# Kernel tuning notes

Hardware: AMD Instinct MI355X
Metric: run time of the kernel (lower is better)

Reference implementation:

```python
import jax, jax.numpy as jnp
import numpy as np

B, C, H, W = 4, 256, 64, 64
TOPK = 3
RAT_S = 0.05  # rat_s passed in Corr.forward


def _zero_window_mask(h, w, rat_s=RAT_S):
    # mask[m, i, j] = 1 - gaussian centered at pixel m=(m//w, m%w); sigma=(h*rat_s, w*rat_s)
    sr, sc = h * rat_s, w * rat_s
    r = jnp.arange(h, dtype=jnp.float32)
    c = jnp.arange(w, dtype=jnp.float32)
    cent_r = jnp.repeat(r, w)  # [hw]
    cent_c = jnp.tile(c, h)    # [hw]
    g = (jnp.exp(-((r[None, :, None] - cent_r[:, None, None]) ** 2) / (2.0 * sr * sr))
         * jnp.exp(-((c[None, None, :] - cent_c[:, None, None]) ** 2) / (2.0 * sc * sc)))
    return (1.0 - g).reshape(h * w, h * w)


def setup_inputs() -> dict:
    key = jax.random.key(0)
    x = jax.random.normal(key, (B, C, H, W), dtype=jnp.float32)
    alpha = jnp.asarray(5.0, dtype=jnp.float32)  # learned scalar nn.Parameter
    return {"x": x, "alpha": alpha}


def reference(x, alpha):
    b, c, h, w = x.shape
    # F.normalize(x, p=2, dim=-3): L2-normalize channels with eps clamp
    nrm = jnp.linalg.norm(x, axis=1, keepdims=True)
    xn = x / jnp.maximum(nrm, 1e-12)
    xf = xn.reshape(b, c, h * w)
    # correlation GEMM: [b, hw, hw]
    aff = jnp.einsum('bcm,bcn->bmn', xf, xf)
    aff = aff * _zero_window_mask(h, w)[None]
    s = aff * alpha
    xc = jax.nn.softmax(s, axis=-1) * jax.nn.softmax(s, axis=-2)
    # topk over the source-pixel dim (dim=-3 of [b, hw, h, w])
    xc = xc.reshape(b, h * w, h, w).transpose(0, 2, 3, 1)  # [b, h, w, hw]
    val, _ = jax.lax.top_k(xc, TOPK)                        # [b, h, w, k]
    return val.transpose(0, 3, 1, 2)                        # [b, k, h, w]
```

## Files before the change

kernel.cpp:

```cpp
#include <hip/hip_runtime.h>
#include <hip/hip_bf16.h>


#define HW 4096
#define CDIM 256
#define INV2S2 0.048828125f
#define NEGINF -1e30f

typedef __bf16 bf16;
typedef __attribute__((ext_vector_type(8))) __bf16 bf16x8;
typedef __attribute__((ext_vector_type(4))) float f32x4;

#define GAS __attribute__((address_space(1)))
#define LAS __attribute__((address_space(3)))

__device__ __forceinline__ void ins3(float v, float& t0, float& t1, float& t2) {
    float n0 = fmaxf(t0, v);
    float n1 = __builtin_amdgcn_fmed3f(t0, t1, v);
    float n2 = __builtin_amdgcn_fmed3f(t1, t2, v);
    t0 = n0; t1 = n1; t2 = n2;
}

__device__ __forceinline__ void decode_tri(int t, int& mt, int& nt) {
    int m = (int)((sqrtf(8.f * (float)t + 1.f) - 1.f) * 0.5f);
    while ((m + 1) * (m + 2) / 2 <= t) ++m;
    while (m * (m + 1) / 2 > t) --m;
    mt = m;
    nt = t - m * (m + 1) / 2;
}

__global__ __launch_bounds__(256) void corr_norm(const float* __restrict__ x,
                                                 bf16* __restrict__ xnT) {
    __shared__ float red[4][64];
    __shared__ float invn[64];
    __shared__ __align__(16) bf16 T[64][264];
    int tid = threadIdx.x;
    int pl = tid & 63, cg = tid >> 6;
    int P0 = blockIdx.x * 64;
    int P = P0 + pl;
    int b = P >> 12;
    int pix = P & 4095;
    const float* xb = x + ((size_t)(b * CDIM + cg * 64) << 12) + pix;
    float v[64];
    float ss = 0.f;
#pragma unroll
    for (int j = 0; j < 64; ++j) {
        v[j] = xb[(size_t)j << 12];
        ss += v[j] * v[j];
    }
    red[cg][pl] = ss;
    __syncthreads();
    if (tid < 64) {
        float s = red[0][tid] + red[1][tid] + red[2][tid] + red[3][tid];
        invn[tid] = 1.0f / fmaxf(sqrtf(s), 1e-12f);
    }
    __syncthreads();
    float inv = invn[pl];
#pragma unroll
    for (int j0 = 0; j0 < 64; j0 += 8) {
        bf16x8 pk;
#pragma unroll
        for (int j = 0; j < 8; ++j) pk[j] = (bf16)(v[j0 + j] * inv);
        *(bf16x8*)(&T[pl][cg * 64 + j0]) = pk;
    }
    __syncthreads();
#pragma unroll
    for (int it = 0; it < 8; ++it) {
        int p = it * 8 + (tid >> 5);
        int k = tid & 31;
        bf16x8 val = *(const bf16x8*)(&T[p][k * 8]);
        *(bf16x8*)(xnT + (size_t)(P0 + p) * CDIM + k * 8) = val;
    }
}

__device__ __forceinline__ void gemm_tile(const bf16* __restrict__ xb, int mbase, int nbase,
                                          bf16* As, bf16* Bs, f32x4 (&acc)[4][4]) {
    const int tid = threadIdx.x;
    const int wave = tid >> 6;
    const int lane = tid & 63;
    const int wm = wave >> 1, wn = wave & 1;
    const int l15 = lane & 15, quad = lane >> 4;
#pragma unroll
    for (int mi = 0; mi < 4; ++mi)
#pragma unroll
        for (int ni = 0; ni < 4; ++ni) acc[mi][ni] = (f32x4)0.f;

    auto issue = [&](int kk, int buf) {
#pragma unroll
        for (int r = 0; r < 2; ++r) {
            int idx = r * 256 + tid;
            int prow = idx >> 2;
            int sub = ((idx & 3) - (prow >> 1)) & 3;
            const bf16* gA = xb + ((size_t)(mbase + prow) << 8) + kk * 32 + (sub << 3);
            const bf16* gB = xb + ((size_t)(nbase + prow) << 8) + kk * 32 + (sub << 3);
            bf16* lA = As + buf * 4096 + ((r * 4 + wave) << 9);
            bf16* lB = Bs + buf * 4096 + ((r * 4 + wave) << 9);
            __builtin_amdgcn_global_load_lds((const GAS void*)gA, (LAS void*)lA, 16, 0, 0);
            __builtin_amdgcn_global_load_lds((const GAS void*)gB, (LAS void*)lB, 16, 0, 0);
        }
    };
    issue(0, 0);
    const int rslot = ((quad + (l15 >> 1)) & 3) * 8;
#pragma unroll
    for (int kk = 0; kk < 8; ++kk) {
        __syncthreads();
        if (kk < 7) issue(kk + 1, (kk + 1) & 1);
        int buf = kk & 1;
        bf16x8 af[4], bfr[4];
#pragma unroll
        for (int i = 0; i < 4; ++i) {
            af[i]  = *(const bf16x8*)(As + buf * 4096 + (wm * 64 + i * 16 + l15) * 32 + rslot);
            bfr[i] = *(const bf16x8*)(Bs + buf * 4096 + (wn * 64 + i * 16 + l15) * 32 + rslot);
        }
#pragma unroll
        for (int mi = 0; mi < 4; ++mi)
#pragma unroll
            for (int ni = 0; ni < 4; ++ni)
                acc[mi][ni] = __builtin_amdgcn_mfma_f32_16x16x32_bf16(af[mi], bfr[ni],
                                                                      acc[mi][ni], 0, 0, 0);
    }
}

__device__ __forceinline__ void build_ext(float* extw, int lane, int adr, float scale) {
    float fr2 = (float)(adr * adr);
#pragma unroll
    for (int h = 0; h < 2; ++h) {
        int j = lane + h * 64;
        float d = (float)(j - 63);
        extw[j] = scale * (1.f - __expf(-(fr2 + d * d) * INV2S2));
    }
}

__device__ __forceinline__ void load_etab(const float* extw_wave, int quad, int l15,
                                          float (&e)[7][4]) {
    const float* p = extw_wave + 63 + quad * 4 - l15;
#pragma unroll
    for (int dm = 0; dm < 7; ++dm)
#pragma unroll
        for (int r = 0; r < 4; ++r) e[dm][r] = p[(dm - 3) * 16 + r];
}

__global__ __launch_bounds__(256) void corr_rowsum(const bf16* __restrict__ xnT,
                                                   const float* __restrict__ alpha_p,
                                                   float* __restrict__ rpart) {
    __shared__ __align__(16) bf16 SH[16384];
    bf16* As = SH;
    bf16* Bs = SH + 8192;
    int tid = threadIdx.x;
    int lin = blockIdx.x;
    int xcd = lin & 7;
    int b = xcd >> 1;
    int t = ((lin >> 3) << 1) + (xcd & 1);
    int mt, nt;
    decode_tri(t, mt, nt);
    int mbase = mt * 128, nbase = nt * 128;
    int wave = tid >> 6, lane = tid & 63;
    int wm = wave >> 1, wn = wave & 1, l15 = lane & 15, quad = lane >> 4;
    int rowi = (mbase + wm * 64) >> 6;
    int coli = (nbase + wn * 64) >> 6;
    int adr = rowi - coli; if (adr < 0) adr = -adr;
    float alpha = alpha_p[0];

    f32x4 acc[4][4];
    gemm_tile(xnT + ((size_t)b << 20), mbase, nbase, As, Bs, acc);

    float* F = (float*)SH;
    float* ext  = F;
    float* rbuf = F + 512;
    float* cbuf = F + 768;
    build_ext(ext + wave * 128, lane, adr, alpha);
    float e[7][4];
    load_etab(ext + wave * 128, quad, l15, e);

    float colpart[4] = {0.f, 0.f, 0.f, 0.f};
#pragma unroll
    for (int mi = 0; mi < 4; ++mi) {
#pragma unroll
        for (int r = 0; r < 4; ++r) {
            float ssum = 0.f;
#pragma unroll
            for (int ni = 0; ni < 4; ++ni) {
                float s = e[mi - ni + 3][r] * acc[mi][ni][r];
                float ev = __expf(s);
                ssum += ev;
                colpart[ni] += ev;
            }
            ssum += __shfl_xor(ssum, 1);
            ssum += __shfl_xor(ssum, 2);
            ssum += __shfl_xor(ssum, 4);
            ssum += __shfl_xor(ssum, 8);
            if (l15 == 0) rbuf[wn * 128 + wm * 64 + mi * 16 + quad * 4 + r] = ssum;
        }
    }
#pragma unroll
    for (int ni = 0; ni < 4; ++ni) {
        float c = colpart[ni];
        c += __shfl_xor(c, 16);
        c += __shfl_xor(c, 32);
        if (quad == 0) cbuf[wm * 128 + wn * 64 + ni * 16 + l15] = c;
    }
    __syncthreads();
    if (tid < 128) {
        rpart[(size_t)((b * 32 + mt) * 32 + nt) * 128 + tid] = rbuf[tid] + rbuf[128 + tid];
    } else if (mt != nt) {
        int j = tid - 128;
        rpart[(size_t)((b * 32 + nt) * 32 + mt) * 128 + j] = cbuf[j] + cbuf[128 + j];
    }
}

__global__ __launch_bounds__(256) void corr_recip(const float* __restrict__ rpart,
                                                  float* __restrict__ ism,
                                                  float* __restrict__ lsm) {
    int i = blockIdx.x * 256 + threadIdx.x;
    if (i >= 4 * HW) return;
    int b = i >> 12, gr = i & 4095, s = gr >> 7, j = gr & 127;
    const float* base = rpart + (size_t)((b * 32 + s) * 32) * 128 + j;
    float sum = 0.f;
#pragma unroll
    for (int sl = 0; sl < 32; ++sl) sum += base[sl * 128];
    ism[i] = 1.0f / sum;
    lsm[i] = -__logf(sum);
}

__global__ __launch_bounds__(256) void corr_topk(const bf16* __restrict__ xnT,
                                                 const float* __restrict__ alpha_p,
                                                 const float* __restrict__ lsm,
                                                 float* __restrict__ wtop) {
    __shared__ __align__(16) bf16 SH[16384];
    bf16* As = SH;
    bf16* Bs = SH + 8192;
    int tid = threadIdx.x;
    int lin = blockIdx.x;
    int xcd = lin & 7;
    int b = xcd >> 1;
    int t = ((lin >> 3) << 1) + (xcd & 1);
    int mt, nt;
    decode_tri(t, mt, nt);
    int mbase = mt * 128, nbase = nt * 128;
    int wave = tid >> 6, lane = tid & 63;
    int wm = wave >> 1, wn = wave & 1, l15 = lane & 15, quad = lane >> 4;
    int rowi = (mbase + wm * 64) >> 6;
    int coli = (nbase + wn * 64) >> 6;
    int adr = rowi - coli; if (adr < 0) adr = -adr;
    float a2 = 2.0f * alpha_p[0];

    f32x4 acc[4][4];
    gemm_tile(xnT + ((size_t)b << 20), mbase, nbase, As, Bs, acc);

    float* F = (float*)SH;
    float* ext  = F;
    float* mbuf = F + 512;
    float* rtop = F + 1280;
    build_ext(ext + wave * 128, lane, adr, a2);
    float e[7][4];
    load_etab(ext + wave * 128, quad, l15, e);

    float lr[4][4];
#pragma unroll
    for (int mi = 0; mi < 4; ++mi)
#pragma unroll
        for (int r = 0; r < 4; ++r)
            lr[mi][r] = lsm[(b << 12) + mbase + wm * 64 + mi * 16 + quad * 4 + r];
    float lc[4];
#pragma unroll
    for (int ni = 0; ni < 4; ++ni)
        lc[ni] = lsm[(b << 12) + nbase + wn * 64 + ni * 16 + l15];

#pragma unroll
    for (int ni = 0; ni < 4; ++ni) {
        float t0 = NEGINF, t1 = NEGINF, t2 = NEGINF;
#pragma unroll
        for (int mi = 0; mi < 4; ++mi) {
#pragma unroll
            for (int r = 0; r < 4; ++r) {
                float key = fmaf(e[mi - ni + 3][r], acc[mi][ni][r], lr[mi][r]);
                ins3(key, t0, t1, t2);
            }
        }
#pragma unroll
        for (int d = 16; d <= 32; d <<= 1) {
            float s0 = __shfl_xor(t0, d);
            float s1 = __shfl_xor(t1, d);
            float s2 = __shfl_xor(t2, d);
            ins3(s0, t0, t1, t2);
            ins3(s1, t0, t1, t2);
            ins3(s2, t0, t1, t2);
        }
        if (quad == 0) {
            int cl = wn * 64 + ni * 16 + l15;
            mbuf[(wm * 128 + cl) * 3 + 0] = t0;
            mbuf[(wm * 128 + cl) * 3 + 1] = t1;
            mbuf[(wm * 128 + cl) * 3 + 2] = t2;
        }
    }
    __syncthreads();

    if (mt != nt) {
#pragma unroll
        for (int mi = 0; mi < 4; ++mi) {
#pragma unroll
            for (int r = 0; r < 4; ++r) {
                float u0 = NEGINF, u1 = NEGINF, u2 = NEGINF;
#pragma unroll
                for (int ni = 0; ni < 4; ++ni) {
                    float key = fmaf(e[mi - ni + 3][r], acc[mi][ni][r], lc[ni]);
                    ins3(key, u0, u1, u2);
                }
                {
                    float s0 = __shfl_xor(u0, 8);
                    float s1 = __shfl_xor(u1, 8);
                    float s2 = __shfl_xor(u2, 8);
                    ins3(s0, u0, u1, u2);
                    ins3(s1, u0, u1, u2);
                    ins3(s2, u0, u1, u2);
                }
                if (l15 < 8) {
                    int row = wm * 64 + mi * 16 + quad * 4 + r;
                    int slot = wn * 8 + l15;
                    float* q = rtop + row * 51 + slot * 3;
                    q[0] = u0; q[1] = u1; q[2] = u2;
                }
            }
        }
    }
    __syncthreads();
    if (tid < 128) {
        float t0 = mbuf[tid * 3], t1 = mbuf[tid * 3 + 1], t2 = mbuf[tid * 3 + 2];
        ins3(mbuf[(128 + tid) * 3 + 0], t0, t1, t2);
        ins3(mbuf[(128 + tid) * 3 + 1], t0, t1, t2);
        ins3(mbuf[(128 + tid) * 3 + 2], t0, t1, t2);
        size_t o = ((size_t)((b * 32 + nt) * 32 + mt) * 128 + tid) * 3;
        wtop[o] = t0;
        wtop[o + 1] = t1;
        wtop[o + 2] = t2;
        if (mt != nt) {
            float v0 = NEGINF, v1 = NEGINF, v2 = NEGINF;
            const float* q = rtop + tid * 51;
#pragma unroll
            for (int sl = 0; sl < 16; ++sl) {
                ins3(q[sl * 3 + 0], v0, v1, v2);
                ins3(q[sl * 3 + 1], v0, v1, v2);
                ins3(q[sl * 3 + 2], v0, v1, v2);
            }
            size_t o2 = ((size_t)((b * 32 + mt) * 32 + nt) * 128 + tid) * 3;
            wtop[o2] = v0;
            wtop[o2 + 1] = v1;
            wtop[o2 + 2] = v2;
        }
    }
}

__global__ __launch_bounds__(256) void corr_merge(const float* __restrict__ wtop,
                                                  const float* __restrict__ ism,
                                                  float* __restrict__ out) {
    int idx = blockIdx.x * 256 + threadIdx.x;
    if (idx >= 4 * HW) return;
    int b = idx >> 12, col = idx & 4095;
    int strip = col >> 7, j = col & 127;
    const float* base = wtop + ((size_t)((b * 32 + strip) * 32) * 128 + j) * 3;
    float t0 = NEGINF, t1 = NEGINF, t2 = NEGINF;
    for (int sl = 0; sl < 32; ++sl) {
        const float* q = base + (size_t)sl * 128 * 3;
        ins3(q[0], t0, t1, t2);
        ins3(q[1], t0, t1, t2);
        ins3(q[2], t0, t1, t2);
    }
    float ismc = ism[idx];
    out[((b * 3 + 0) << 12) + col] = __expf(t0) * ismc;
    out[((b * 3 + 1) << 12) + col] = __expf(t1) * ismc;
    out[((b * 3 + 2) << 12) + col] = __expf(t2) * ismc;
}

extern "C" void kernel_launch(void* const* d_in, const int* in_sizes, int n_in,
                              void* d_out, int out_size, void* d_ws, size_t ws_size,
                              hipStream_t stream) {
    const float* x = (const float*)d_in[0];
    const float* alpha = (const float*)d_in[1];
    float* out = (float*)d_out;
    char* ws = (char*)d_ws;
    bf16* xnT = (bf16*)ws;
    float* ism = (float*)(ws + (8u << 20));
    float* lsm = (float*)(ws + (8u << 20) + (64u << 10));
    float* rpart = (float*)(ws + (8u << 20) + (128u << 10));
    float* wtop  = (float*)(ws + (8u << 20) + (128u << 10));

    corr_norm<<<256, 256, 0, stream>>>(x, xnT);
    corr_rowsum<<<528 * 4, 256, 0, stream>>>(xnT, alpha, rpart);
    corr_recip<<<64, 256, 0, stream>>>(rpart, ism, lsm);
    corr_topk<<<528 * 4, 256, 0, stream>>>(xnT, alpha, lsm, wtop);
    corr_merge<<<64, 256, 0, stream>>>(wtop, ism, out);
}
```

Before: 155.0 us.

## Fuse five kernels into one persistent kernel with global atomic barriers

```diff
diff --git a/kernel.cpp b/kernel.cpp
--- a/kernel.cpp
+++ b/kernel.cpp
@@ -6,6 +6,9 @@
 #define CDIM 256
 #define INV2S2 0.048828125f
 #define NEGINF -1e30f
+#define NTILE 528
+#define NWORK_GEMM (NTILE * 4)
+#define GRID 512
 
 typedef __bf16 bf16;
 typedef __attribute__((ext_vector_type(8))) __bf16 bf16x8;
@@ -19,6 +22,18 @@
     float n1 = __builtin_amdgcn_fmed3f(t0, t1, v);
     float n2 = __builtin_amdgcn_fmed3f(t1, t2, v);
     t0 = n0; t1 = n1; t2 = n2;
+}
+
+__device__ __forceinline__ void gbarrier(int* cnt, int target) {
+    __syncthreads();
+    if (threadIdx.x == 0) {
+        __threadfence();
+        __hip_atomic_fetch_add(cnt, 1, __ATOMIC_RELEASE, __HIP_MEMORY_SCOPE_AGENT);
+        while (__hip_atomic_load(cnt, __ATOMIC_ACQUIRE, __HIP_MEMORY_SCOPE_AGENT) < target)
+            __builtin_amdgcn_s_sleep(8);
+        __threadfence();
+    }
+    __syncthreads();
 }
 
 __device__ __forceinline__ void decode_tri(int t, int& mt, int& nt) {
@@ -27,50 +42,6 @@
     while (m * (m + 1) / 2 > t) --m;
     mt = m;
     nt = t - m * (m + 1) / 2;
-}
-
-__global__ __launch_bounds__(256) void corr_norm(const float* __restrict__ x,
-                                                 bf16* __restrict__ xnT) {
-    __shared__ float red[4][64];
-    __shared__ float invn[64];
-    __shared__ __align__(16) bf16 T[64][264];
-    int tid = threadIdx.x;
-    int pl = tid & 63, cg = tid >> 6;
-    int P0 = blockIdx.x * 64;
-    int P = P0 + pl;
-    int b = P >> 12;
-    int pix = P & 4095;
-    const float* xb = x + ((size_t)(b * CDIM + cg * 64) << 12) + pix;
-    float v[64];
-    float ss = 0.f;
-#pragma unroll
-    for (int j = 0; j < 64; ++j) {
-        v[j] = xb[(size_t)j << 12];
-        ss += v[j] * v[j];
-    }
-    red[cg][pl] = ss;
-    __syncthreads();
-    if (tid < 64) {
-        float s = red[0][tid] + red[1][tid] + red[2][tid] + red[3][tid];
-        invn[tid] = 1.0f / fmaxf(sqrtf(s), 1e-12f);
-    }
-    __syncthreads();
-    float inv = invn[pl];
-#pragma unroll
-    for (int j0 = 0; j0 < 64; j0 += 8) {
-        bf16x8 pk;
-#pragma unroll
-        for (int j = 0; j < 8; ++j) pk[j] = (bf16)(v[j0 + j] * inv);
-        *(bf16x8*)(&T[pl][cg * 64 + j0]) = pk;
-    }
-    __syncthreads();
-#pragma unroll
-    for (int it = 0; it < 8; ++it) {
-        int p = it * 8 + (tid >> 5);
-        int k = tid & 31;
-        bf16x8 val = *(const bf16x8*)(&T[p][k * 8]);
-        *(bf16x8*)(xnT + (size_t)(P0 + p) * CDIM + k * 8) = val;
-    }
 }
 
 __device__ __forceinline__ void gemm_tile(const bf16* __restrict__ xb, int mbase, int nbase,
@@ -140,14 +111,64 @@
         for (int r = 0; r < 4; ++r) e[dm][r] = p[(dm - 3) * 16 + r];
 }
 
-__global__ __launch_bounds__(256) void corr_rowsum(const bf16* __restrict__ xnT,
-                                                   const float* __restrict__ alpha_p,
-                                                   float* __restrict__ rpart) {
-    __shared__ __align__(16) bf16 SH[16384];
+__device__ __forceinline__ void norm_phase(int wid, const float* __restrict__ x,
+                                           bf16* __restrict__ xnT, bf16* SH) {
+    float* F = (float*)SH;
+    float* red  = F;
+    float* invn = F + 256;
+    bf16* T = SH + 4096;
+    int tid = threadIdx.x;
+    int pl = tid & 63, cg = tid >> 6;
+    int P0 = wid * 64;
+    int P = P0 + pl;
+    int b = P >> 12;
+    int pix = P & 4095;
+    const float* xb = x + ((size_t)(b * CDIM + cg * 64) << 12) + pix;
+    float v[64];
+    float ss = 0.f;
+#pragma unroll
+    for (int j = 0; j < 64; ++j) {
+        v[j] = xb[(size_t)j << 12];
+        ss += v[j] * v[j];
+    }
+    red[cg * 64 + pl] = ss;
+    __syncthreads();
+    if (tid < 64) {
+        float s = red[tid] + red[64 + tid] + red[128 + tid] + red[192 + tid];
+        invn[tid] = 1.0f / fmaxf(sqrtf(s), 1e-12f);
+    }
+    __syncthreads();
+    float inv = invn[pl];
+#pragma unroll
+    for (int h = 0; h < 2; ++h) {
+        if ((cg >> 1) == h) {
+            int base = (cg & 1) * 64;
+#pragma unroll
+            for (int j0 = 0; j0 < 64; j0 += 8) {
+                bf16x8 pk;
+#pragma unroll
+                for (int j = 0; j < 8; ++j) pk[j] = (bf16)(v[j0 + j] * inv);
+                *(bf16x8*)(T + pl * 136 + base + j0) = pk;
+            }
+        }
+        __syncthreads();
+#pragma unroll
+        for (int it = 0; it < 4; ++it) {
+            int p = it * 16 + (tid >> 4);
+            int k = tid & 15;
+            bf16x8 val = *(const bf16x8*)(T + p * 136 + k * 8);
+            *(bf16x8*)(xnT + (size_t)(P0 + p) * CDIM + h * 128 + k * 8) = val;
+        }
+        __syncthreads();
+    }
+}
+
+__device__ __forceinline__ void rowsum_phase(int lin, const bf16* __restrict__ xnT,
+                                             const float* __restrict__ alpha_p,
+                                             float* __restrict__ rpart, bf16* SH) {
     bf16* As = SH;
     bf16* Bs = SH + 8192;
     int tid = threadIdx.x;
-    int lin = blockIdx.x;
     int xcd = lin & 7;
     int b = xcd >> 1;
     int t = ((lin >> 3) << 1) + (xcd & 1);
@@ -206,13 +227,12 @@
         int j = tid - 128;
         rpart[(size_t)((b * 32 + nt) * 32 + mt) * 128 + j] = cbuf[j] + cbuf[128 + j];
     }
-}
-
-__global__ __launch_bounds__(256) void corr_recip(const float* __restrict__ rpart,
-                                                  float* __restrict__ ism,
-                                                  float* __restrict__ lsm) {
-    int i = blockIdx.x * 256 + threadIdx.x;
-    if (i >= 4 * HW) return;
+    __syncthreads();
+}
+
+__device__ __forceinline__ void recip_phase(int wid, const float* __restrict__ rpart,
+                                            float* __restrict__ ism, float* __restrict__ lsm) {
+    int i = wid * 256 + threadIdx.x;
     int b = i >> 12, gr = i & 4095, s = gr >> 7, j = gr & 127;
     const float* base = rpart + (size_t)((b * 32 + s) * 32) * 128 + j;
     float sum = 0.f;
@@ -222,15 +242,13 @@
     lsm[i] = -__logf(sum);
 }
 
-__global__ __launch_bounds__(256) void corr_topk(const bf16* __restrict__ xnT,
-                                                 const float* __restrict__ alpha_p,
-                                                 const float* __restrict__ lsm,
-                                                 float* __restrict__ wtop) {
-    __shared__ __align__(16) bf16 SH[16384];
+__device__ __forceinline__ void topk_phase(int lin, const bf16* __restrict__ xnT,
+                                           const float* __restrict__ alpha_p,
+                                           const float* __restrict__ lsm,
+                                           float* __restrict__ wtop, bf16* SH) {
     bf16* As = SH;
     bf16* Bs = SH + 8192;
     int tid = threadIdx.x;
-    int lin = blockIdx.x;
     int xcd = lin & 7;
     int b = xcd >> 1;
     int t = ((lin >> 3) << 1) + (xcd & 1);
@@ -348,13 +366,13 @@
             wtop[o2 + 2] = v2;
         }
     }
-}
-
-__global__ __launch_bounds__(256) void corr_merge(const float* __restrict__ wtop,
-                                                  const float* __restrict__ ism,
-                                                  float* __restrict__ out) {
-    int idx = blockIdx.x * 256 + threadIdx.x;
-    if (idx >= 4 * HW) return;
+    __syncthreads();
+}
+
+__device__ __forceinline__ void merge_phase(int wid, const float* __restrict__ wtop,
+                                            const float* __restrict__ ism,
+                                            float* __restrict__ out) {
+    int idx = wid * 256 + threadIdx.x;
     int b = idx >> 12, col = idx & 4095;
     int strip = col >> 7, j = col & 127;
     const float* base = wtop + ((size_t)((b * 32 + strip) * 32) * 128 + j) * 3;
@@ -369,6 +387,27 @@
     out[((b * 3 + 0) << 12) + col] = __expf(t0) * ismc;
     out[((b * 3 + 1) << 12) + col] = __expf(t1) * ismc;
     out[((b * 3 + 2) << 12) + col] = __expf(t2) * ismc;
+}
+
+__global__ __launch_bounds__(256, 2) void corr_all(const float* __restrict__ x,
+                                                   const float* __restrict__ alpha_p,
+                                                   bf16* __restrict__ xnT,
+                                                   float* __restrict__ rpart,
+                                                   float* __restrict__ ism,
+                                                   float* __restrict__ lsm,
+                                                   float* __restrict__ wtop,
+                                                   float* __restrict__ out,
+                                                   int* __restrict__ cnt) {
+    __shared__ __align__(16) bf16 SH[16384];
+    for (int w = blockIdx.x; w < 256; w += GRID) norm_phase(w, x, xnT, SH);
+    gbarrier(cnt, 1 * GRID);
+    for (int w = blockIdx.x; w < NWORK_GEMM; w += GRID) rowsum_phase(w, xnT, alpha_p, rpart, SH);
+    gbarrier(cnt, 2 * GRID);
+    for (int w = blockIdx.x; w < 64; w += GRID) recip_phase(w, rpart, ism, lsm);
+    gbarrier(cnt, 3 * GRID);
+    for (int w = blockIdx.x; w < NWORK_GEMM; w += GRID) topk_phase(w, xnT, alpha_p, lsm, wtop, SH);
+    gbarrier(cnt, 4 * GRID);
+    for (int w = blockIdx.x; w < 64; w += GRID) merge_phase(w, wtop, ism, out);
 }
 
 extern "C" void kernel_launch(void* const* d_in, const int* in_sizes, int n_in,
@@ -383,10 +422,8 @@
     float* lsm = (float*)(ws + (8u << 20) + (64u << 10));
     float* rpart = (float*)(ws + (8u << 20) + (128u << 10));
     float* wtop  = (float*)(ws + (8u << 20) + (128u << 10));
-
-    corr_norm<<<256, 256, 0, stream>>>(x, xnT);
-    corr_rowsum<<<528 * 4, 256, 0, stream>>>(xnT, alpha, rpart);
-    corr_recip<<<64, 256, 0, stream>>>(rpart, ism, lsm);
-    corr_topk<<<528 * 4, 256, 0, stream>>>(xnT, alpha, lsm, wtop);
-    corr_merge<<<64, 256, 0, stream>>>(wtop, ism, out);
-}
+    int* cnt = (int*)(ws + (8u << 20) + (128u << 10) + (6u << 20));
+
+    hipMemsetAsync(cnt, 0, 64, stream);
+    corr_all<<<GRID, 256, 0, stream>>>(x, alpha, xnT, rpart, ism, lsm, wtop, out, cnt);
+}
```

Result: slower. 460.1 us (+196.9%).

## Fuse row-sum reciprocal and top-k merge into GEMM kernels via last-block atomic counters

Applied to the files above, without the earlier changes.

```diff
diff --git a/kernel.cpp b/kernel.cpp
--- a/kernel.cpp
+++ b/kernel.cpp
@@ -6,6 +6,7 @@
 #define CDIM 256
 #define INV2S2 0.048828125f
 #define NEGINF -1e30f
+#define NTILE 528
 
 typedef __bf16 bf16;
 typedef __attribute__((ext_vector_type(8))) __bf16 bf16x8;
@@ -142,8 +143,12 @@
 
 __global__ __launch_bounds__(256) void corr_rowsum(const bf16* __restrict__ xnT,
                                                    const float* __restrict__ alpha_p,
-                                                   float* __restrict__ rpart) {
+                                                   float* __restrict__ rpart,
+                                                   float* __restrict__ ism,
+                                                   float* __restrict__ lsm,
+                                                   int* __restrict__ cnt) {
     __shared__ __align__(16) bf16 SH[16384];
+    __shared__ int fin0, fin1;
     bf16* As = SH;
     bf16* Bs = SH + 8192;
     int tid = threadIdx.x;
@@ -206,27 +211,54 @@
         int j = tid - 128;
         rpart[(size_t)((b * 32 + nt) * 32 + mt) * 128 + j] = cbuf[j] + cbuf[128 + j];
     }
-}
-
-__global__ __launch_bounds__(256) void corr_recip(const float* __restrict__ rpart,
-                                                  float* __restrict__ ism,
-                                                  float* __restrict__ lsm) {
-    int i = blockIdx.x * 256 + threadIdx.x;
-    if (i >= 4 * HW) return;
-    int b = i >> 12, gr = i & 4095, s = gr >> 7, j = gr & 127;
-    const float* base = rpart + (size_t)((b * 32 + s) * 32) * 128 + j;
-    float sum = 0.f;
-#pragma unroll
-    for (int sl = 0; sl < 32; ++sl) sum += base[sl * 128];
-    ism[i] = 1.0f / sum;
-    lsm[i] = -__logf(sum);
+    __syncthreads();
+    if (tid == 0) {
+        __threadfence();
+        int oa = __hip_atomic_fetch_add(&cnt[b * 32 + mt], 1, __ATOMIC_RELAXED,
+                                        __HIP_MEMORY_SCOPE_AGENT);
+        int f0 = (oa == 31);
+        int f1 = 0;
+        if (mt != nt) {
+            int ob = __hip_atomic_fetch_add(&cnt[b * 32 + nt], 1, __ATOMIC_RELAXED,
+                                            __HIP_MEMORY_SCOPE_AGENT);
+            f1 = (ob == 31);
+        }
+        if (f0 | f1) __threadfence();
+        fin0 = f0;
+        fin1 = f1;
+    }
+    __syncthreads();
+    if (tid < 128) {
+        if (fin0) {
+            int i = (b << 12) + mt * 128 + tid;
+            const float* base = rpart + (size_t)((b * 32 + mt) * 32) * 128 + tid;
+            float sum = 0.f;
+#pragma unroll
+            for (int sl = 0; sl < 32; ++sl) sum += base[sl * 128];
+            ism[i] = 1.0f / sum;
+            lsm[i] = -__logf(sum);
+        }
+        if (fin1) {
+            int i = (b << 12) + nt * 128 + tid;
+            const float* base = rpart + (size_t)((b * 32 + nt) * 32) * 128 + tid;
+            float sum = 0.f;
+#pragma unroll
+            for (int sl = 0; sl < 32; ++sl) sum += base[sl * 128];
+            ism[i] = 1.0f / sum;
+            lsm[i] = -__logf(sum);
+        }
+    }
 }
 
 __global__ __launch_bounds__(256) void corr_topk(const bf16* __restrict__ xnT,
                                                  const float* __restrict__ alpha_p,
                                                  const float* __restrict__ lsm,
-                                                 float* __restrict__ wtop) {
+                                                 const float* __restrict__ ism,
+                                                 float* __restrict__ wtop,
+                                                 float* __restrict__ out,
+                                                 int* __restrict__ cnt) {
     __shared__ __align__(16) bf16 SH[16384];
+    __shared__ int fin0, fin1;
     bf16* As = SH;
     bf16* Bs = SH + 8192;
     int tid = threadIdx.x;
@@ -348,27 +380,44 @@
             wtop[o2 + 2] = v2;
         }
     }
-}
-
-__global__ __launch_bounds__(256) void corr_merge(const float* __restrict__ wtop,
-                                                  const float* __restrict__ ism,
-                                                  float* __restrict__ out) {
-    int idx = blockIdx.x * 256 + threadIdx.x;
-    if (idx >= 4 * HW) return;
-    int b = idx >> 12, col = idx & 4095;
-    int strip = col >> 7, j = col & 127;
-    const float* base = wtop + ((size_t)((b * 32 + strip) * 32) * 128 + j) * 3;
-    float t0 = NEGINF, t1 = NEGINF, t2 = NEGINF;
-    for (int sl = 0; sl < 32; ++sl) {
-        const float* q = base + (size_t)sl * 128 * 3;
-        ins3(q[0], t0, t1, t2);
-        ins3(q[1], t0, t1, t2);
-        ins3(q[2], t0, t1, t2);
-    }
-    float ismc = ism[idx];
-    out[((b * 3 + 0) << 12) + col] = __expf(t0) * ismc;
-    out[((b * 3 + 1) << 12) + col] = __expf(t1) * ismc;
-    out[((b * 3 + 2) << 12) + col] = __expf(t2) * ismc;
+    __syncthreads();
+    if (tid == 0) {
+        __threadfence();
+        int oa = __hip_atomic_fetch_add(&cnt[b * 32 + nt], 1, __ATOMIC_RELAXED,
+                                        __HIP_MEMORY_SCOPE_AGENT);
+        int f0 = (oa == 31);
+        int f1 = 0;
+        if (mt != nt) {
+            int ob = __hip_atomic_fetch_add(&cnt[b * 32 + mt], 1, __ATOMIC_RELAXED,
+                                            __HIP_MEMORY_SCOPE_AGENT);
+            f1 = (ob == 31);
+        }
+        if (f0 | f1) __threadfence();
+        fin0 = f0;
+        fin1 = f1;
+    }
+    __syncthreads();
+    if (tid < 128) {
+        for (int pass = 0; pass < 2; ++pass) {
+            int s = pass == 0 ? nt : mt;
+            int go = pass == 0 ? fin0 : fin1;
+            if (!go) continue;
+            int idx = (b << 12) + s * 128 + tid;
+            const float* base = wtop + ((size_t)((b * 32 + s) * 32) * 128 + tid) * 3;
+            float t0 = NEGINF, t1 = NEGINF, t2 = NEGINF;
+            for (int sl = 0; sl < 32; ++sl) {
+                const float* q = base + (size_t)sl * 128 * 3;
+                ins3(q[0], t0, t1, t2);
+                ins3(q[1], t0, t1, t2);
+                ins3(q[2], t0, t1, t2);
+            }
+            float ismc = ism[idx];
+            int col = s * 128 + tid;
+            out[((b * 3 + 0) << 12) + col] = __expf(t0) * ismc;
+            out[((b * 3 + 1) << 12) + col] = __expf(t1) * ismc;
+            out[((b * 3 + 2) << 12) + col] = __expf(t2) * ismc;
+        }
+    }
 }
 
 extern "C" void kernel_launch(void* const* d_in, const int* in_sizes, int n_in,
@@ -383,10 +432,11 @@
     float* lsm = (float*)(ws + (8u << 20) + (64u << 10));
     float* rpart = (float*)(ws + (8u << 20) + (128u << 10));
     float* wtop  = (float*)(ws + (8u << 20) + (128u << 10));
-
+    int* cntA = (int*)(ws + (8u << 20) + (128u << 10) + (6u << 20));
+    int* cntB = cntA + 128;
+
+    hipMemsetAsync(cntA, 0, 256 * sizeof(int), stream);
     corr_norm<<<256, 256, 0, stream>>>(x, xnT);
-    corr_rowsum<<<528 * 4, 256, 0, stream>>>(xnT, alpha, rpart);
-    corr_recip<<<64, 256, 0, stream>>>(rpart, ism, lsm);
-    corr_topk<<<528 * 4, 256, 0, stream>>>(xnT, alpha, lsm, wtop);
-    corr_merge<<<64, 256, 0, stream>>>(wtop, ism, out);
-}
+    corr_rowsum<<<NTILE * 4, 256, 0, stream>>>(xnT, alpha, rpart, ism, lsm, cntA);
+    corr_topk<<<NTILE * 4, 256, 0, stream>>>(xnT, alpha, lsm, ism, wtop, out, cntB);
+}
```

Result: slower. 260.5 us (+68.1%).

## Store scaled scores as fp16 in rowsum pass and skip GEMM recompute in topk

Applied to the files above, without the earlier changes.

```diff
diff --git a/kernel.cpp b/kernel.cpp
--- a/kernel.cpp
+++ b/kernel.cpp
@@ -6,9 +6,12 @@
 #define CDIM 256
 #define INV2S2 0.048828125f
 #define NEGINF -1e30f
+#define NTILE 528
 
 typedef __bf16 bf16;
+typedef _Float16 f16;
 typedef __attribute__((ext_vector_type(8))) __bf16 bf16x8;
+typedef __attribute__((ext_vector_type(4))) _Float16 f16x4;
 typedef __attribute__((ext_vector_type(4))) float f32x4;
 
 #define GAS __attribute__((address_space(1)))
@@ -142,7 +145,9 @@
 
 __global__ __launch_bounds__(256) void corr_rowsum(const bf16* __restrict__ xnT,
                                                    const float* __restrict__ alpha_p,
-                                                   float* __restrict__ rpart) {
+                                                   float* __restrict__ rpart,
+                                                   f16* __restrict__ sbuf,
+                                                   int store_s2) {
     __shared__ __align__(16) bf16 SH[16384];
     bf16* As = SH;
     bf16* Bs = SH + 8192;
@@ -172,18 +177,27 @@
     float e[7][4];
     load_etab(ext + wave * 128, quad, l15, e);
 
+    const size_t tb = (size_t)(b * NTILE + t) * 16384;
     float colpart[4] = {0.f, 0.f, 0.f, 0.f};
 #pragma unroll
     for (int mi = 0; mi < 4; ++mi) {
 #pragma unroll
         for (int r = 0; r < 4; ++r) {
             float ssum = 0.f;
+            float sv[4];
 #pragma unroll
             for (int ni = 0; ni < 4; ++ni) {
                 float s = e[mi - ni + 3][r] * acc[mi][ni][r];
+                sv[ni] = s;
                 float ev = __expf(s);
                 ssum += ev;
                 colpart[ni] += ev;
+            }
+            if (store_s2) {
+                f16x4 pk;
+#pragma unroll
+                for (int ni = 0; ni < 4; ++ni) pk[ni] = (f16)(sv[ni] + sv[ni]);
+                *(f16x4*)(sbuf + tb + (mi * 4 + r) * 1024 + tid * 4) = pk;
             }
             ssum += __shfl_xor(ssum, 1);
             ssum += __shfl_xor(ssum, 2);
@@ -220,6 +234,134 @@
     for (int sl = 0; sl < 32; ++sl) sum += base[sl * 128];
     ism[i] = 1.0f / sum;
     lsm[i] = -__logf(sum);
+}
+
+__device__ __forceinline__ void topk_epilogue(int b, int mt, int nt,
+                                              const float (&s2f)[16][4],
+                                              const float (&lr)[4][4], const float (&lc)[4],
+                                              float* mbuf, float* rtop,
+                                              float* __restrict__ wtop,
+                                              int tid, int wm, int wn, int l15, int quad) {
+#pragma unroll
+    for (int ni = 0; ni < 4; ++ni) {
+        float t0 = NEGINF, t1 = NEGINF, t2 = NEGINF;
+#pragma unroll
+        for (int mi = 0; mi < 4; ++mi) {
+#pragma unroll
+            for (int r = 0; r < 4; ++r) {
+                float key = s2f[mi * 4 + r][ni] + lr[mi][r];
+                ins3(key, t0, t1, t2);
+            }
+        }
+#pragma unroll
+        for (int d = 16; d <= 32; d <<= 1) {
+            float s0 = __shfl_xor(t0, d);
+            float s1 = __shfl_xor(t1, d);
+            float s2 = __shfl_xor(t2, d);
+            ins3(s0, t0, t1, t2);
+            ins3(s1, t0, t1, t2);
+            ins3(s2, t0, t1, t2);
+        }
+        if (quad == 0) {
+            int cl = wn * 64 + ni * 16 + l15;
+            mbuf[(wm * 128 + cl) * 3 + 0] = t0;
+            mbuf[(wm * 128 + cl) * 3 + 1] = t1;
+            mbuf[(wm * 128 + cl) * 3 + 2] = t2;
+        }
+    }
+    __syncthreads();
+    if (mt != nt) {
+#pragma unroll
+        for (int mi = 0; mi < 4; ++mi) {
+#pragma unroll
+            for (int r = 0; r < 4; ++r) {
+                float u0 = NEGINF, u1 = NEGINF, u2 = NEGINF;
+#pragma unroll
+                for (int ni = 0; ni < 4; ++ni) {
+                    float key = s2f[mi * 4 + r][ni] + lc[ni];
+                    ins3(key, u0, u1, u2);
+                }
+                {
+                    float s0 = __shfl_xor(u0, 8);
+                    float s1 = __shfl_xor(u1, 8);
+                    float s2 = __shfl_xor(u2, 8);
+                    ins3(s0, u0, u1, u2);
+                    ins3(s1, u0, u1, u2);
+                    ins3(s2, u0, u1, u2);
+                }
+                if (l15 < 8) {
+                    int row = wm * 64 + mi * 16 + quad * 4 + r;
+                    int slot = wn * 8 + l15;
+                    float* q = rtop + row * 51 + slot * 3;
+                    q[0] = u0; q[1] = u1; q[2] = u2;
+                }
+            }
+        }
+    }
+    __syncthreads();
+    if (tid < 128) {
+        float t0 = mbuf[tid * 3], t1 = mbuf[tid * 3 + 1], t2 = mbuf[tid * 3 + 2];
+        ins3(mbuf[(128 + tid) * 3 + 0], t0, t1, t2);
+        ins3(mbuf[(128 + tid) * 3 + 1], t0, t1, t2);
+        ins3(mbuf[(128 + tid) * 3 + 2], t0, t1, t2);
+        size_t o = ((size_t)((b * 32 + nt) * 32 + mt) * 128 + tid) * 3;
+        wtop[o] = t0;
+        wtop[o + 1] = t1;
+        wtop[o + 2] = t2;
+        if (mt != nt) {
+            float v0 = NEGINF, v1 = NEGINF, v2 = NEGINF;
+            const float* q = rtop + tid * 51;
+#pragma unroll
+            for (int sl = 0; sl < 16; ++sl) {
+                ins3(q[sl * 3 + 0], v0, v1, v2);
+                ins3(q[sl * 3 + 1], v0, v1, v2);
+                ins3(q[sl * 3 + 2], v0, v1, v2);
+            }
+            size_t o2 = ((size_t)((b * 32 + mt) * 32 + nt) * 128 + tid) * 3;
+            wtop[o2] = v0;
+            wtop[o2 + 1] = v1;
+            wtop[o2 + 2] = v2;
+        }
+    }
+}
+
+__global__ __launch_bounds__(256) void corr_topsel(const f16* __restrict__ sbuf,
+                                                   const float* __restrict__ lsm,
+                                                   float* __restrict__ wtop) {
+    __shared__ float FS[7296];
+    float* mbuf = FS;
+    float* rtop = FS + 768;
+    int tid = threadIdx.x;
+    int lin = blockIdx.x;
+    int xcd = lin & 7;
+    int b = xcd >> 1;
+    int t = ((lin >> 3) << 1) + (xcd & 1);
+    int mt, nt;
+    decode_tri(t, mt, nt);
+    int mbase = mt * 128, nbase = nt * 128;
+    int wave = tid >> 6, lane = tid & 63;
+    int wm = wave >> 1, wn = wave & 1, l15 = lane & 15, quad = lane >> 4;
+
+    const size_t tb = (size_t)(b * NTILE + t) * 16384;
+    float s2f[16][4];
+#pragma unroll
+    for (int k = 0; k < 16; ++k) {
+        f16x4 hv = *(const f16x4*)(sbuf + tb + k * 1024 + tid * 4);
+#pragma unroll
+        for (int ni = 0; ni < 4; ++ni) s2f[k][ni] = (float)hv[ni];
+    }
+    float lr[4][4];
+#pragma unroll
+    for (int mi = 0; mi < 4; ++mi)
+#pragma unroll
+        for (int r = 0; r < 4; ++r)
+            lr[mi][r] = lsm[(b << 12) + mbase + wm * 64 + mi * 16 + quad * 4 + r];
+    float lc[4];
+#pragma unroll
+    for (int ni = 0; ni < 4; ++ni)
+        lc[ni] = lsm[(b << 12) + nbase + wn * 64 + ni * 16 + l15];
+
+    topk_epilogue(b, mt, nt, s2f, lr, lc, mbuf, rtop, wtop, tid, wm, wn, l15, quad);
 }
 
 __global__ __launch_bounds__(256) void corr_topk(const bf16* __restrict__ xnT,
@@ -255,6 +397,14 @@
     float e[7][4];
     load_etab(ext + wave * 128, quad, l15, e);
 
+    float s2f[16][4];
+#pragma unroll
+    for (int mi = 0; mi < 4; ++mi)
+#pragma unroll
+        for (int r = 0; r < 4; ++r)
+#pragma unroll
+            for (int ni = 0; ni < 4; ++ni)
+                s2f[mi * 4 + r][ni] = e[mi - ni + 3][r] * acc[mi][ni][r];
     float lr[4][4];
 #pragma unroll
     for (int mi = 0; mi < 4; ++mi)
@@ -266,88 +416,8 @@
     for (int ni = 0; ni < 4; ++ni)
         lc[ni] = lsm[(b << 12) + nbase + wn * 64 + ni * 16 + l15];
 
-#pragma unroll
-    for (int ni = 0; ni < 4; ++ni) {
-        float t0 = NEGINF, t1 = NEGINF, t2 = NEGINF;
-#pragma unroll
-        for (int mi = 0; mi < 4; ++mi) {
-#pragma unroll
-            for (int r = 0; r < 4; ++r) {
-                float key = fmaf(e[mi - ni + 3][r], acc[mi][ni][r], lr[mi][r]);
-                ins3(key, t0, t1, t2);
-            }
-        }
-#pragma unroll
-        for (int d = 16; d <= 32; d <<= 1) {
-            float s0 = __shfl_xor(t0, d);
-            float s1 = __shfl_xor(t1, d);
-            float s2 = __shfl_xor(t2, d);
-            ins3(s0, t0, t1, t2);
-            ins3(s1, t0, t1, t2);
-            ins3(s2, t0, t1, t2);
-        }
-        if (quad == 0) {
-            int cl = wn * 64 + ni * 16 + l15;
-            mbuf[(wm * 128 + cl) * 3 + 0] = t0;
-            mbuf[(wm * 128 + cl) * 3 + 1] = t1;
-            mbuf[(wm * 128 + cl) * 3 + 2] = t2;
-        }
-    }
-    __syncthreads();
-
-    if (mt != nt) {
-#pragma unroll
-        for (int mi = 0; mi < 4; ++mi) {
-#pragma unroll
-            for (int r = 0; r < 4; ++r) {
-                float u0 = NEGINF, u1 = NEGINF, u2 = NEGINF;
-#pragma unroll
-                for (int ni = 0; ni < 4; ++ni) {
-                    float key = fmaf(e[mi - ni + 3][r], acc[mi][ni][r], lc[ni]);
-                    ins3(key, u0, u1, u2);
-                }
-                {
-                    float s0 = __shfl_xor(u0, 8);
-                    float s1 = __shfl_xor(u1, 8);
-                    float s2 = __shfl_xor(u2, 8);
-                    ins3(s0, u0, u1, u2);
-                    ins3(s1, u0, u1, u2);
-                    ins3(s2, u0, u1, u2);
-                }
-                if (l15 < 8) {
-                    int row = wm * 64 + mi * 16 + quad * 4 + r;
-                    int slot = wn * 8 + l15;
-                    float* q = rtop + row * 51 + slot * 3;
-                    q[0] = u0; q[1] = u1; q[2] = u2;
-                }
-            }
-        }
-    }
-    __syncthreads();
-    if (tid < 128) {
-        float t0 = mbuf[tid * 3], t1 = mbuf[tid * 3 + 1], t2 = mbuf[tid * 3 + 2];
-        ins3(mbuf[(128 + tid) * 3 + 0], t0, t1, t2);
-        ins3(mbuf[(128 + tid) * 3 + 1], t0, t1, t2);
-        ins3(mbuf[(128 + tid) * 3 + 2], t0, t1, t2);
-        size_t o = ((size_t)((b * 32 + nt) * 32 + mt) * 128 + tid) * 3;
-        wtop[o] = t0;
-        wtop[o + 1] = t1;
-        wtop[o + 2] = t2;
-        if (mt != nt) {
-            float v0 = NEGINF, v1 = NEGINF, v2 = NEGINF;
-            const float* q = rtop + tid * 51;
-#pragma unroll
-            for (int sl = 0; sl < 16; ++sl) {
-                ins3(q[sl * 3 + 0], v0, v1, v2);
-                ins3(q[sl * 3 + 1], v0, v1, v2);
-                ins3(q[sl * 3 + 2], v0, v1, v2);
-            }
-            size_t o2 = ((size_t)((b * 32 + mt) * 32 + nt) * 128 + tid) * 3;
-            wtop[o2] = v0;
-            wtop[o2 + 1] = v1;
-            wtop[o2 + 2] = v2;
-        }
-    }
+    __syncthreads();
+    topk_epilogue(b, mt, nt, s2f, lr, lc, mbuf, rtop, wtop, tid, wm, wn, l15, quad);
 }
 
 __global__ __launch_bounds__(256) void corr_merge(const float* __restrict__ wtop,
@@ -383,10 +453,16 @@
     float* lsm = (float*)(ws + (8u << 20) + (64u << 10));
     float* rpart = (float*)(ws + (8u << 20) + (128u << 10));
     float* wtop  = (float*)(ws + (8u << 20) + (128u << 10));
+    f16* sbuf = (f16*)(ws + (8u << 20) + (128u << 10) + (6u << 20));
+    size_t need = (8u << 20) + (128u << 10) + (6u << 20) + (size_t)4 * NTILE * 16384 * 2;
+    int fast = (ws_size >= need);
 
     corr_norm<<<256, 256, 0, stream>>>(x, xnT);
-    corr_rowsum<<<528 * 4, 256, 0, stream>>>(xnT, alpha, rpart);
+    corr_rowsum<<<NTILE * 4, 256, 0, stream>>>(xnT, alpha, rpart, sbuf, fast);
     corr_recip<<<64, 256, 0, stream>>>(rpart, ism, lsm);
-    corr_topk<<<528 * 4, 256, 0, stream>>>(xnT, alpha, lsm, wtop);
+    if (fast)
+        corr_topsel<<<NTILE * 4, 256, 0, stream>>>(sbuf, lsm, wtop);
+    else
+        corr_topk<<<NTILE * 4, 256, 0, stream>>>(xnT, alpha, lsm, wtop);
     corr_merge<<<64, 256, 0, stream>>>(wtop, ism, out);
 }
```

Measured after the change: 140.5 us. 1.1x faster.
